# Optimization experiments

Measured on AMD Instinct MI355X. Metric: run time of the kernel, lower is better.

The kernel has to match this reference:

```python
import jax, jax.numpy as jnp
import numpy as np

V, E, G, D = 30000, 60000, 1200, 64
NODE_IN, EDGE_IN, EH = 74, 12, 128
N_MP, N_S2S, N_LSTM = 6, 6, 3


def setup_inputs() -> dict:
    key = jax.random.key(0)
    ks = iter(jax.random.split(key, 48))
    def rn(shape, s=0.05):
        return jax.random.normal(next(ks), shape, dtype=jnp.float32) * s
    inp = {
        "node_feats": jax.random.normal(next(ks), (V, NODE_IN), dtype=jnp.float32),
        "edge_feats": jax.random.normal(next(ks), (E, EDGE_IN), dtype=jnp.float32),
        "src": jax.random.randint(next(ks), (E,), 0, V, dtype=jnp.int32),
        "dst": jax.random.randint(next(ks), (E,), 0, V, dtype=jnp.int32),
        "node_graph_ids": jnp.sort(jax.random.randint(next(ks), (V,), 0, G, dtype=jnp.int32)),
        # MPNNGNN: node projection, edge network, NNConv bias, GRU
        "proj_W": rn((NODE_IN, D)), "proj_b": rn((D,)),
        "eW1": rn((EDGE_IN, EH)), "eb1": rn((EH,)),
        "eW2": rn((EH, D * D)), "eb2": rn((D * D,)),
        "conv_b": rn((D,)),
        "gru_Wih": rn((D, 3 * D)), "gru_bih": rn((3 * D,)),
        "gru_Whh": rn((D, 3 * D)), "gru_bhh": rn((3 * D,)),
        # process + predict MLPs
        "pW": rn((2 * D, D)), "pb": rn((D,)),
        "qW1": rn((D, D)), "qb1": rn((D,)),
        "qW2": rn((D, D)), "qb2": rn((D,)),
        "qW3": rn((D, 1)), "qb3": rn((1,)),
    }
    # Set2Set 3-layer LSTM: layer0 input 2D, layers 1-2 input D; gates i,f,g,o
    for l, din in enumerate([2 * D, D, D]):
        inp[f"lstm_Wih{l}"] = rn((din, 4 * D)); inp[f"lstm_bih{l}"] = rn((4 * D,))
        inp[f"lstm_Whh{l}"] = rn((D, 4 * D)); inp[f"lstm_bhh{l}"] = rn((4 * D,))
    return inp


def _forward(floats, src, dst, gids):
    (node_feats, edge_feats, proj_W, proj_b, eW1, eb1, eW2, eb2, conv_b,
     gru_Wih, gru_bih, gru_Whh, gru_bhh,
     lWih0, lbih0, lWhh0, lbhh0,
     lWih1, lbih1, lWhh1, lbhh1,
     lWih2, lbih2, lWhh2, lbhh2,
     pW, pb, qW1, qb1, qW2, qb2, qW3, qb3) = floats

    # ---- MPNNGNN ----
    h = jax.nn.relu(node_feats @ proj_W + proj_b)            # (V, D)
    hidden = h
    # per-edge weight matrices (edge_feats fixed across MP steps -> compute once)
    We = (jax.nn.relu(edge_feats @ eW1 + eb1) @ eW2 + eb2).reshape(E, D, D)
    for _ in range(N_MP):
        m = jnp.einsum('ei,eio->eo', h[src], We)             # (E, D)
        agg = jax.ops.segment_sum(m, dst, num_segments=V) + conv_b
        x = jax.nn.relu(agg)
        # PyTorch GRU cell
        gi = x @ gru_Wih + gru_bih
        gh = hidden @ gru_Whh + gru_bhh
        ir, iz, inn = jnp.split(gi, 3, axis=-1)
        hr, hz, hn = jnp.split(gh, 3, axis=-1)
        r = jax.nn.sigmoid(ir + hr)
        z = jax.nn.sigmoid(iz + hz)
        n = jnp.tanh(inn + r * hn)
        h = (1.0 - z) * n + z * hidden
        hidden = h

    # ---- Set2Set readout ----
    lstm = [(lWih0, lbih0, lWhh0, lbhh0),
            (lWih1, lbih1, lWhh1, lbhh1),
            (lWih2, lbih2, lWhh2, lbhh2)]
    hs = [jnp.zeros((G, D), h.dtype) for _ in range(N_LSTM)]
    cs = [jnp.zeros((G, D), h.dtype) for _ in range(N_LSTM)]
    q_star = jnp.zeros((G, 2 * D), h.dtype)
    for _ in range(N_S2S):
        x = q_star
        nhs, ncs = [], []
        for l, (Wih, bih, Whh, bhh) in enumerate(lstm):
            gates = x @ Wih + bih + hs[l] @ Whh + bhh
            i_g, f_g, g_g, o_g = jnp.split(gates, 4, axis=-1)
            c = jax.nn.sigmoid(f_g) * cs[l] + jax.nn.sigmoid(i_g) * jnp.tanh(g_g)
            hh = jax.nn.sigmoid(o_g) * jnp.tanh(c)
            nhs.append(hh); ncs.append(c)
            x = hh
        hs, cs = nhs, ncs
        q = x                                               # (G, D)
        e = jnp.sum(h * q[gids], axis=-1)                   # (V,)
        emax = jax.ops.segment_max(e, gids, num_segments=G, indices_are_sorted=True)
        ex = jnp.exp(e - emax[gids])
        denom = jax.ops.segment_sum(ex, gids, num_segments=G, indices_are_sorted=True)
        alpha = ex / denom[gids]                            # per-graph softmax
        readout = jax.ops.segment_sum(h * alpha[:, None], gids, num_segments=G, indices_are_sorted=True)
        q_star = jnp.concatenate([q, readout], axis=-1)     # (G, 2D)

    # ---- process + predict MLPs (dropout = identity in eval) ----
    gf = jax.nn.relu(q_star @ pW + pb)
    y = jax.nn.relu(gf @ qW1 + qb1)
    y = jax.nn.relu(y @ qW2 + qb2)
    return y @ qW3 + qb3                                    # (G, 1)


def reference(node_feats, edge_feats, src, dst, node_graph_ids,
              proj_W, proj_b, eW1, eb1, eW2, eb2, conv_b,
              gru_Wih, gru_bih, gru_Whh, gru_bhh,
              lstm_Wih0, lstm_bih0, lstm_Whh0, lstm_bhh0,
              lstm_Wih1, lstm_bih1, lstm_Whh1, lstm_bhh1,
              lstm_Wih2, lstm_bih2, lstm_Whh2, lstm_bhh2,
              pW, pb, qW1, qb1, qW2, qb2, qW3, qb3):
    floats = (node_feats, edge_feats, proj_W, proj_b, eW1, eb1, eW2, eb2, conv_b,
              gru_Wih, gru_bih, gru_Whh, gru_bhh,
              lstm_Wih0, lstm_bih0, lstm_Whh0, lstm_bhh0,
              lstm_Wih1, lstm_bih1, lstm_Whh1, lstm_bhh1,
              lstm_Wih2, lstm_bih2, lstm_Whh2, lstm_bhh2,
              pW, pb, qW1, qb1, qW2, qb2, qW3, qb3)
    return _forward(floats, src, dst, node_graph_ids)
```

## Files before the change

kernel.cpp:

```cpp
#include <hip/hip_runtime.h>
#include <stdint.h>
#include <math.h>

#define V 30000
#define E 60000
#define G 1200
#define D 64
#define NODE_IN 74
#define EDGE_IN 12
#define EH 128
#define N_MP 6
#define N_S2S 6

#define NBLK ((E + 63) / 64)
#define EPAD (NBLK * 64)
#define GRUBLK ((V + 31) / 32)

typedef short bf16x8 __attribute__((ext_vector_type(8)));
typedef float f32x4 __attribute__((ext_vector_type(4)));

__device__ __forceinline__ float sigmoidf_(float x) {
    return 1.0f / (1.0f + __expf(-x));
}
__device__ __forceinline__ float tanhf_(float x) {
    float t = __expf(-2.0f * fabsf(x));
    float r = (1.0f - t) / (1.0f + t);
    return copysignf(r, x);
}
__device__ __forceinline__ uint16_t f2bf(float f) {
    uint32_t u = __float_as_uint(f);
    u += 0x7fffu + ((u >> 16) & 1u);
    return (uint16_t)(u >> 16);
}
__device__ __forceinline__ float bf2f(uint16_t u) {
    return __uint_as_float(((uint32_t)u) << 16);
}

__global__ void k_zero(float* __restrict__ p, int n4) {
    int i = blockIdx.x * blockDim.x + threadIdx.x;
    if (i < n4) ((float4*)p)[i] = make_float4(0.f, 0.f, 0.f, 0.f);
}

__global__ void k_node_proj(const float* __restrict__ nf, const float* __restrict__ W,
                            const float* __restrict__ b, float* __restrict__ h) {
    int wave = threadIdx.x >> 6, lane = threadIdx.x & 63;
    int v = blockIdx.x * 4 + wave;
    __shared__ float xs[4][NODE_IN];
    xs[wave][lane] = nf[(size_t)v * NODE_IN + lane];
    if (lane + 64 < NODE_IN) xs[wave][lane + 64] = nf[(size_t)v * NODE_IN + lane + 64];
    __syncthreads();
    float acc = b[lane];
    #pragma unroll
    for (int i = 0; i < NODE_IN; ++i) acc = fmaf(xs[wave][i], W[i * D + lane], acc);
    h[(size_t)v * D + lane] = fmaxf(acc, 0.0f);
}

__global__ __launch_bounds__(256) void k_edge_hidden(const float* __restrict__ ef,
                              const float* __restrict__ W1,
                              const float* __restrict__ b1, uint16_t* __restrict__ HedgeP) {
    int blk = blockIdx.x;
    int t = threadIdx.x;
    int half = t >> 7, j = t & 127;
    __shared__ float xs[8][EDGE_IN];
    if (t < 8 * EDGE_IN) {
        int el = t / EDGE_IN, c = t % EDGE_IN;
        int e = blk * 8 + el;
        xs[el][c] = (e < E) ? ef[(size_t)e * EDGE_IN + c] : 0.f;
    }
    __syncthreads();
    #pragma unroll
    for (int l = 0; l < 4; ++l) {
        int el = half * 4 + l;
        int e = blk * 8 + el;
        float acc = b1[j];
        #pragma unroll
        for (int i = 0; i < EDGE_IN; ++i) acc = fmaf(xs[el][i], W1[i * EH + j], acc);
        float r = (e < E) ? fmaxf(acc, 0.0f) : 0.0f;
        int bb = e >> 6, ww = (e >> 4) & 3, m = e & 15;
        int kt = j >> 5, quad = (j >> 3) & 3, jj = j & 7;
        size_t off = ((((size_t)(bb * 4 + ww) * 4 + kt) * 4 + quad) * 16 + m) * 8 + jj;
        HedgeP[off] = f2bf(r);
    }
}

__global__ void k_prep_w2(const float* __restrict__ eW2, uint16_t* __restrict__ W2p) {
    int idx = blockIdx.x * 256 + threadIdx.x;
    int j = idx & 7;
    int n0 = (idx >> 3) & 15;
    int quad = (idx >> 7) & 3;
    int nt = (idx >> 9) & 3;
    int kt = (idx >> 11) & 3;
    int i = idx >> 13;
    int k = kt * 32 + quad * 8 + j;
    int col = i * 64 + nt * 16 + n0;
    W2p[idx] = f2bf(eW2[(size_t)k * 4096 + col]);
}

__global__ void k_prep_b2(const float* __restrict__ eb2, uint16_t* __restrict__ B2p) {
    int idx = blockIdx.x * 256 + threadIdx.x;
    if (idx >= 4096) { B2p[idx] = 0; return; }
    int j = idx & 7;
    int n0 = (idx >> 3) & 15;
    int quad = (idx >> 7) & 3;
    int nt = (idx >> 9) & 3;
    int kb = (idx >> 11) & 1;
    B2p[idx] = f2bf(eb2[(size_t)(kb * 32 + quad * 8 + j) * 64 + nt * 16 + n0]);
}

__global__ void k_prep_wc(const float* __restrict__ Wih, const float* __restrict__ Whh,
                          const float* __restrict__ bih, const float* __restrict__ bhh,
                          uint16_t* __restrict__ Wcp, float* __restrict__ bc) {
    int idx = blockIdx.x * 256 + threadIdx.x;
    int j = idx & 7;
    int n0 = (idx >> 3) & 15;
    int quad = (idx >> 7) & 3;
    int kt = (idx >> 9) & 3;
    int ot = idx >> 11;
    int k = kt * 32 + quad * 8 + j;
    int c = ot * 16 + n0;
    float val = 0.f;
    if (c < 128) {
        val = (k < 64) ? Wih[(size_t)k * 192 + c] : Whh[(size_t)(k - 64) * 192 + c];
    } else if (c < 192) {
        if (k < 64) val = Wih[(size_t)k * 192 + c];
    } else {
        if (k >= 64) val = Whh[(size_t)(k - 64) * 192 + (c - 64)];
    }
    Wcp[idx] = f2bf(val);
    if (idx < 256) {
        int d = idx & 63;
        float b;
        if (idx < 64)       b = bih[d] + bhh[d];
        else if (idx < 128) b = bih[64 + d] + bhh[64 + d];
        else if (idx < 192) b = bih[128 + d];
        else                b = bhh[128 + d];
        bc[idx] = b;
    }
}

__global__ __launch_bounds__(256, 3) void k_message_mfma(
    const uint16_t* __restrict__ HedgeP, const uint16_t* __restrict__ W2p,
    const uint16_t* __restrict__ B2p, const float* __restrict__ h,
    const int* __restrict__ src, const int* __restrict__ dst,
    float* __restrict__ agg) {
    const int bx = blockIdx.x;
    const int b = bx >> 1;
    const int ibase = (bx & 1) * 32;
    const int t = threadIdx.x;
    const int w = t >> 6, lane = t & 63;
    const int quad = lane >> 4, n0 = lane & 15;

    __shared__ uint16_t HsU[64][72];
    __shared__ int srcv[64], dstv[64];

    if (t < 64) {
        int e = b * 64 + t;
        int sv = 0, dv = -1;
        if (e < E) { sv = src[e]; dv = dst[e]; }
        srcv[t] = sv; dstv[t] = dv;
    }
    __syncthreads();
    for (int idx = t; idx < 4096; idx += 256) {
        int r = idx >> 6, c = idx & 63;
        HsU[r][c] = f2bf(h[(size_t)srcv[r] * 64 + c]);
    }
    bf16x8 Af[4][4];
    #pragma unroll
    for (int et = 0; et < 4; ++et)
        #pragma unroll
        for (int kt = 0; kt < 4; ++kt)
            Af[et][kt] = *(const bf16x8*)(HedgeP + (((size_t)(b * 4 + et) * 4 + kt) * 512) + lane * 8);
    __syncthreads();

    f32x4 acc[4];
    {
        const uint16_t* b2b = B2p + (size_t)ibase * 128;
        bf16x8 B2f0 = *(const bf16x8*)(b2b + (size_t)(0 * 4 + w) * 512 + lane * 8);
        bf16x8 B2f1 = *(const bf16x8*)(b2b + (size_t)(1 * 4 + w) * 512 + lane * 8);
        #pragma unroll
        for (int et = 0; et < 4; ++et) {
            bf16x8 hA0 = *(const bf16x8*)(&HsU[et * 16 + n0][quad * 8]);
            bf16x8 hA1 = *(const bf16x8*)(&HsU[et * 16 + n0][32 + quad * 8]);
            f32x4 z = {};
            z = __builtin_amdgcn_mfma_f32_16x16x32_bf16(hA0, B2f0, z, 0, 0, 0);
            acc[et] = __builtin_amdgcn_mfma_f32_16x16x32_bf16(hA1, B2f1, z, 0, 0, 0);
        }
    }

    for (int ii = 0; ii < 32; ++ii) {
        const int i = ibase + ii;
        const uint16_t* wb = W2p + (size_t)i * 8192 + lane * 8;
        bf16x8 Bf0 = *(const bf16x8*)(wb + (size_t)(0 * 4 + w) * 512);
        bf16x8 Bf1 = *(const bf16x8*)(wb + (size_t)(1 * 4 + w) * 512);
        bf16x8 Bf2 = *(const bf16x8*)(wb + (size_t)(2 * 4 + w) * 512);
        bf16x8 Bf3 = *(const bf16x8*)(wb + (size_t)(3 * 4 + w) * 512);
        #pragma unroll
        for (int et = 0; et < 4; ++et) {
            f32x4 tmp = {};
            tmp = __builtin_amdgcn_mfma_f32_16x16x32_bf16(Af[et][0], Bf0, tmp, 0, 0, 0);
            tmp = __builtin_amdgcn_mfma_f32_16x16x32_bf16(Af[et][1], Bf1, tmp, 0, 0, 0);
            tmp = __builtin_amdgcn_mfma_f32_16x16x32_bf16(Af[et][2], Bf2, tmp, 0, 0, 0);
            tmp = __builtin_amdgcn_mfma_f32_16x16x32_bf16(Af[et][3], Bf3, tmp, 0, 0, 0);
            int r0 = et * 16 + quad * 4;
            acc[et][0] = fmaf(bf2f(HsU[r0 + 0][i]), tmp[0], acc[et][0]);
            acc[et][1] = fmaf(bf2f(HsU[r0 + 1][i]), tmp[1], acc[et][1]);
            acc[et][2] = fmaf(bf2f(HsU[r0 + 2][i]), tmp[2], acc[et][2]);
            acc[et][3] = fmaf(bf2f(HsU[r0 + 3][i]), tmp[3], acc[et][3]);
        }
    }

    #pragma unroll
    for (int et = 0; et < 4; ++et) {
        #pragma unroll
        for (int reg = 0; reg < 4; ++reg) {
            int d = dstv[et * 16 + quad * 4 + reg];
            if (d >= 0)
                atomicAdd(agg + (size_t)d * 64 + w * 16 + n0, acc[et][reg]);
        }
    }
}

__global__ __launch_bounds__(256) void k_gru_mfma(
    float* __restrict__ agg, const float* __restrict__ convb,
    const uint16_t* __restrict__ Wcp, const float* __restrict__ bc,
    float* __restrict__ hcur) {
    const int blk = blockIdx.x;
    const int v0 = blk * 32;
    const int t = threadIdx.x;
    const int w = t >> 6, lane = t & 63;
    const int quad = lane >> 4, n0 = lane & 15;

    __shared__ uint16_t As[32][136];
    __shared__ uint16_t Gs[32][264];

    for (int idx = t; idx < 2048; idx += 256) {
        int r = idx >> 6, c = idx & 63;
        int v = v0 + r;
        if (v < V) {
            size_t off = (size_t)v * 64 + c;
            float x = fmaxf(agg[off] + convb[c], 0.f);
            agg[off] = 0.f;
            As[r][c] = f2bf(x);
            As[r][64 + c] = f2bf(hcur[off]);
        } else {
            As[r][c] = 0; As[r][64 + c] = 0;
        }
    }
    __syncthreads();

    bf16x8 Af[2][4];
    #pragma unroll
    for (int et = 0; et < 2; ++et)
        #pragma unroll
        for (int kt = 0; kt < 4; ++kt)
            Af[et][kt] = *(const bf16x8*)(&As[et * 16 + n0][kt * 32 + quad * 8]);

    f32x4 acc[2][4] = {};
    #pragma unroll
    for (int ot4 = 0; ot4 < 4; ++ot4) {
        const uint16_t* wb = Wcp + (size_t)((w * 4 + ot4) * 4) * 512 + lane * 8;
        bf16x8 B0 = *(const bf16x8*)(wb + 0 * 512);
        bf16x8 B1 = *(const bf16x8*)(wb + 1 * 512);
        bf16x8 B2 = *(const bf16x8*)(wb + 2 * 512);
        bf16x8 B3 = *(const bf16x8*)(wb + 3 * 512);
        #pragma unroll
        for (int et = 0; et < 2; ++et) {
            f32x4 a = acc[et][ot4];
            a = __builtin_amdgcn_mfma_f32_16x16x32_bf16(Af[et][0], B0, a, 0, 0, 0);
            a = __builtin_amdgcn_mfma_f32_16x16x32_bf16(Af[et][1], B1, a, 0, 0, 0);
            a = __builtin_amdgcn_mfma_f32_16x16x32_bf16(Af[et][2], B2, a, 0, 0, 0);
            a = __builtin_amdgcn_mfma_f32_16x16x32_bf16(Af[et][3], B3, a, 0, 0, 0);
            acc[et][ot4] = a;
        }
    }
    #pragma unroll
    for (int et = 0; et < 2; ++et)
        #pragma unroll
        for (int ot4 = 0; ot4 < 4; ++ot4)
            #pragma unroll
            for (int reg = 0; reg < 4; ++reg)
                Gs[et * 16 + quad * 4 + reg][(w * 4 + ot4) * 16 + n0] = f2bf(acc[et][ot4][reg]);
    __syncthreads();

    for (int idx = t; idx < 2048; idx += 256) {
        int r = idx >> 6, d = idx & 63;
        int v = v0 + r;
        if (v >= V) continue;
        size_t off = (size_t)v * 64 + d;
        float rp   = bf2f(Gs[r][d])        + bc[d];
        float zp   = bf2f(Gs[r][64 + d])   + bc[64 + d];
        float innv = bf2f(Gs[r][128 + d])  + bc[128 + d];
        float hnv  = bf2f(Gs[r][192 + d])  + bc[192 + d];
        float hv = hcur[off];
        float rr = sigmoidf_(rp);
        float zz = sigmoidf_(zp);
        float nn = tanhf_(innv + rr * hnv);
        hcur[off] = (1.f - zz) * nn + zz * hv;
    }
}

__global__ void k_seg(const int* __restrict__ gids, int* __restrict__ start) {
    int v = blockIdx.x * blockDim.x + threadIdx.x;
    if (v > V) return;
    int cur = (v < V) ? gids[v] : G;
    int prev = (v == 0) ? -1 : gids[v - 1];
    for (int g = prev + 1; g <= cur; ++g) start[g] = v;
}

#define LS_GPB 8
__global__ __launch_bounds__(256) void k_s2s_final(
    const float* __restrict__ h, const int* __restrict__ segs,
    const float* __restrict__ Wih0, const float* __restrict__ bih0,
    const float* __restrict__ Whh0, const float* __restrict__ bhh0,
    const float* __restrict__ Wih1, const float* __restrict__ bih1,
    const float* __restrict__ Whh1, const float* __restrict__ bhh1,
    const float* __restrict__ Wih2, const float* __restrict__ bih2,
    const float* __restrict__ Whh2, const float* __restrict__ bhh2,
    const float* __restrict__ pW, const float* __restrict__ pb,
    const float* __restrict__ qW1, const float* __restrict__ qb1,
    const float* __restrict__ qW2, const float* __restrict__ qb2,
    const float* __restrict__ qW3, const float* __restrict__ qb3,
    float* __restrict__ out) {
    const int g0 = blockIdx.x * LS_GPB;
    const int j = threadIdx.x;
    const int w = j >> 6, lane = j & 63;

    __shared__ float xs[LS_GPB][128];
    __shared__ float hsL[3][LS_GPB][64];
    __shared__ float csL[3][LS_GPB][64];
    __shared__ float gates[LS_GPB][256];
    __shared__ float qst[LS_GPB][128];

    for (int idx = j; idx < LS_GPB * 64 * 3; idx += 256) {
        ((float*)hsL)[idx] = 0.f;
        ((float*)csL)[idx] = 0.f;
    }
    for (int idx = j; idx < LS_GPB * 128; idx += 256) ((float*)qst)[idx] = 0.f;
    __syncthreads();

    const float* Wihs[3] = {Wih0, Wih1, Wih2};
    const float* bihs[3] = {bih0, bih1, bih2};
    const float* Whhs[3] = {Whh0, Whh1, Whh2};
    const float* bhhs[3] = {bhh0, bhh1, bhh2};
    const int dins[3] = {128, 64, 64};

    for (int s = 0; s < N_S2S; ++s) {
        for (int idx = j; idx < LS_GPB * 128; idx += 256) {
            int n = idx >> 7, d = idx & 127;
            xs[n][d] = qst[n][d];
        }
        __syncthreads();
        for (int l = 0; l < 3; ++l) {
            float acc[LS_GPB];
            float bsum = bihs[l][j] + bhhs[l][j];
            #pragma unroll
            for (int n = 0; n < LS_GPB; ++n) acc[n] = bsum;
            const float* Wih = Wihs[l];
            int din = dins[l];
            for (int i = 0; i < din; ++i) {
                float wv = Wih[i * 256 + j];
                #pragma unroll
                for (int n = 0; n < LS_GPB; ++n) acc[n] = fmaf(xs[n][i], wv, acc[n]);
            }
            const float* Whh = Whhs[l];
            for (int i = 0; i < 64; ++i) {
                float wv = Whh[i * 256 + j];
                #pragma unroll
                for (int n = 0; n < LS_GPB; ++n) acc[n] = fmaf(hsL[l][n][i], wv, acc[n]);
            }
            #pragma unroll
            for (int n = 0; n < LS_GPB; ++n) gates[n][j] = acc[n];
            __syncthreads();
            for (int idx = j; idx < LS_GPB * 64; idx += 256) {
                int n = idx >> 6, d = idx & 63;
                float ig = gates[n][d], fg = gates[n][64 + d];
                float gt = gates[n][128 + d], og = gates[n][192 + d];
                float c = sigmoidf_(fg) * csL[l][n][d] + sigmoidf_(ig) * tanhf_(gt);
                float hnew = sigmoidf_(og) * tanhf_(c);
                csL[l][n][d] = c;
                hsL[l][n][d] = hnew;
                xs[n][d] = hnew;
            }
            __syncthreads();
        }
        #pragma unroll
        for (int gi = 0; gi < 2; ++gi) {
            int gg = w + gi * 4;
            int g = g0 + gg;
            float qd = xs[gg][lane];
            int vs = segs[g], ve = segs[g + 1];
            float m = -INFINITY, sden = 0.f, accd = 0.f;
            for (int v = vs; v < ve; ++v) {
                float hv = h[(size_t)v * 64 + lane];
                float p = hv * qd;
                #pragma unroll
                for (int off = 32; off > 0; off >>= 1) p += __shfl_xor(p, off, 64);
                float nm = fmaxf(m, p);
                float e1 = __expf(m - nm);
                float e2 = __expf(p - nm);
                sden = sden * e1 + e2;
                accd = accd * e1 + hv * e2;
                m = nm;
            }
            float r = (ve > vs) ? accd / sden : 0.f;
            qst[gg][lane] = qd;
            qst[gg][64 + lane] = r;
        }
        __syncthreads();
    }

    #pragma unroll
    for (int gi = 0; gi < 2; ++gi) {
        int gg = w + gi * 4;
        int g = g0 + gg;
        float y = pb[lane];
        for (int i = 0; i < 128; ++i) y = fmaf(qst[gg][i], pW[i * 64 + lane], y);
        y = fmaxf(y, 0.f);
        gates[gg][lane] = y;
        float y1 = qb1[lane];
        for (int i = 0; i < 64; ++i) y1 = fmaf(gates[gg][i], qW1[i * 64 + lane], y1);
        y1 = fmaxf(y1, 0.f);
        gates[gg][64 + lane] = y1;
        float y2 = qb2[lane];
        for (int i = 0; i < 64; ++i) y2 = fmaf(gates[gg][64 + i], qW2[i * 64 + lane], y2);
        y2 = fmaxf(y2, 0.f);
        float p = y2 * qW3[lane];
        #pragma unroll
        for (int off = 32; off > 0; off >>= 1) p += __shfl_xor(p, off, 64);
        if (lane == 0) out[g] = p + qb3[0];
    }
}

extern "C" void kernel_launch(void* const* d_in, const int* in_sizes, int n_in,
                              void* d_out, int out_size, void* d_ws, size_t ws_size,
                              hipStream_t stream) {
    const float* node_feats = (const float*)d_in[0];
    const float* edge_feats = (const float*)d_in[1];
    const int*   src        = (const int*)d_in[2];
    const int*   dst        = (const int*)d_in[3];
    const int*   gids       = (const int*)d_in[4];
    const float* proj_W     = (const float*)d_in[5];
    const float* proj_b     = (const float*)d_in[6];
    const float* eW1        = (const float*)d_in[7];
    const float* eb1        = (const float*)d_in[8];
    const float* eW2        = (const float*)d_in[9];
    const float* eb2        = (const float*)d_in[10];
    const float* conv_b     = (const float*)d_in[11];
    const float* gru_Wih    = (const float*)d_in[12];
    const float* gru_bih    = (const float*)d_in[13];
    const float* gru_Whh    = (const float*)d_in[14];
    const float* gru_bhh    = (const float*)d_in[15];
    const float* pW         = (const float*)d_in[16];
    const float* pb         = (const float*)d_in[17];
    const float* qW1        = (const float*)d_in[18];
    const float* qb1        = (const float*)d_in[19];
    const float* qW2        = (const float*)d_in[20];
    const float* qb2        = (const float*)d_in[21];
    const float* qW3        = (const float*)d_in[22];
    const float* qb3        = (const float*)d_in[23];
    const float* lWih0 = (const float*)d_in[24]; const float* lbih0 = (const float*)d_in[25];
    const float* lWhh0 = (const float*)d_in[26]; const float* lbhh0 = (const float*)d_in[27];
    const float* lWih1 = (const float*)d_in[28]; const float* lbih1 = (const float*)d_in[29];
    const float* lWhh1 = (const float*)d_in[30]; const float* lbhh1 = (const float*)d_in[31];
    const float* lWih2 = (const float*)d_in[32]; const float* lbih2 = (const float*)d_in[33];
    const float* lWhh2 = (const float*)d_in[34]; const float* lbhh2 = (const float*)d_in[35];

    char* ws = (char*)d_ws;
    uint16_t* HedgeP = (uint16_t*)(ws + 0);
    uint16_t* W2p    = (uint16_t*)(ws + 15368192);
    uint16_t* B2p    = (uint16_t*)(ws + 16416768);
    float*    hcur   = (float*)(ws + 16433152);
    float*    agg    = (float*)(ws + 24113152);
    int*      segs   = (int*)(ws + 34557952);
    uint16_t* Wcp    = (uint16_t*)(ws + 32407552);
    float*    bc     = (float*)(ws + 32407552 + 65536);

    k_node_proj<<<V / 4, 256, 0, stream>>>(node_feats, proj_W, proj_b, hcur);
    k_edge_hidden<<<EPAD / 8, 256, 0, stream>>>(edge_feats, eW1, eb1, HedgeP);
    k_prep_w2<<<2048, 256, 0, stream>>>(eW2, W2p);
    k_prep_b2<<<32, 256, 0, stream>>>(eb2, B2p);
    k_prep_wc<<<128, 256, 0, stream>>>(gru_Wih, gru_Whh, gru_bih, gru_bhh, Wcp, bc);
    k_seg<<<(V + 1 + 255) / 256, 256, 0, stream>>>(gids, segs);
    k_zero<<<(480000 + 255) / 256, 256, 0, stream>>>(agg, 480000);

    for (int t = 0; t < N_MP; ++t) {
        k_message_mfma<<<NBLK * 2, 256, 0, stream>>>(HedgeP, W2p, B2p, hcur, src, dst, agg);
        k_gru_mfma<<<GRUBLK, 256, 0, stream>>>(agg, conv_b, Wcp, bc, hcur);
    }

    k_s2s_final<<<G / LS_GPB, 256, 0, stream>>>(hcur, segs,
        lWih0, lbih0, lWhh0, lbhh0,
        lWih1, lbih1, lWhh1, lbhh1,
        lWih2, lbih2, lWhh2, lbhh2,
        pW, pb, qW1, qb1, qW2, qb2, qW3, qb3,
        (float*)d_out);
}
```

Before: 954.0 us.

## Run Set2Set LSTM with one wavefront per graph using shuffles and packed gate weights

Rewrites the Set2Set/readout kernel to process one graph per 64-thread block. Each lane owns one hidden unit and computes all four LSTM gates from float4-packed weights that a new prep kernel interleaves. Inputs are broadcast with wave shuffles instead of shared memory, which removes block-wide syncs and lets 1200 blocks spread across the GPU instead of 150. The cost is that each graph re-reads the full LSTM weights with no reuse across graphs, so weight traffic per block rises.

```diff
diff --git a/kernel.cpp b/kernel.cpp
--- a/kernel.cpp
+++ b/kernel.cpp
@@ -138,6 +138,42 @@
     }
 }
 
+__global__ void k_prep_lstm(
+    const float* __restrict__ Wih0, const float* __restrict__ bih0,
+    const float* __restrict__ Whh0, const float* __restrict__ bhh0,
+    const float* __restrict__ Wih1, const float* __restrict__ bih1,
+    const float* __restrict__ Whh1, const float* __restrict__ bhh1,
+    const float* __restrict__ Wih2, const float* __restrict__ bih2,
+    const float* __restrict__ Whh2, const float* __restrict__ bhh2,
+    float4* __restrict__ WihP, float4* __restrict__ WhhP, float4* __restrict__ bc4) {
+    int idx = blockIdx.x * 256 + threadIdx.x;
+    if (idx < 16384) {
+        const float* W; int base;
+        if (idx < 8192)       { base = 0;     W = Wih0; }
+        else if (idx < 12288) { base = 8192;  W = Wih1; }
+        else                  { base = 12288; W = Wih2; }
+        int local = idx - base;
+        int i = local >> 6, d = local & 63;
+        WihP[idx] = make_float4(W[(size_t)i * 256 + d],       W[(size_t)i * 256 + 64 + d],
+                                W[(size_t)i * 256 + 128 + d], W[(size_t)i * 256 + 192 + d]);
+    } else if (idx < 28672) {
+        int li = idx - 16384;
+        int l = li >> 12;
+        int local = li & 4095;
+        int k = local >> 6, d = local & 63;
+        const float* W = (l == 0) ? Whh0 : (l == 1) ? Whh1 : Whh2;
+        WhhP[li] = make_float4(W[(size_t)k * 256 + d],       W[(size_t)k * 256 + 64 + d],
+                               W[(size_t)k * 256 + 128 + d], W[(size_t)k * 256 + 192 + d]);
+    } else if (idx < 28864) {
+        int bi = idx - 28672;
+        int l = bi >> 6, d = bi & 63;
+        const float* bi_ = (l == 0) ? bih0 : (l == 1) ? bih1 : bih2;
+        const float* bh_ = (l == 0) ? bhh0 : (l == 1) ? bhh1 : bhh2;
+        bc4[bi] = make_float4(bi_[d] + bh_[d],             bi_[64 + d] + bh_[64 + d],
+                              bi_[128 + d] + bh_[128 + d], bi_[192 + d] + bh_[192 + d]);
+    }
+}
+
 __global__ __launch_bounds__(256, 3) void k_message_mfma(
     const uint16_t* __restrict__ HedgeP, const uint16_t* __restrict__ W2p,
     const uint16_t* __restrict__ B2p, const float* __restrict__ h,
@@ -307,128 +343,122 @@
     for (int g = prev + 1; g <= cur; ++g) start[g] = v;
 }
 
-#define LS_GPB 8
-__global__ __launch_bounds__(256) void k_s2s_final(
+__global__ __launch_bounds__(64) void k_s2s_final(
     const float* __restrict__ h, const int* __restrict__ segs,
-    const float* __restrict__ Wih0, const float* __restrict__ bih0,
-    const float* __restrict__ Whh0, const float* __restrict__ bhh0,
-    const float* __restrict__ Wih1, const float* __restrict__ bih1,
-    const float* __restrict__ Whh1, const float* __restrict__ bhh1,
-    const float* __restrict__ Wih2, const float* __restrict__ bih2,
-    const float* __restrict__ Whh2, const float* __restrict__ bhh2,
+    const float4* __restrict__ WihP, const float4* __restrict__ WhhP,
+    const float4* __restrict__ bc4,
     const float* __restrict__ pW, const float* __restrict__ pb,
     const float* __restrict__ qW1, const float* __restrict__ qb1,
     const float* __restrict__ qW2, const float* __restrict__ qb2,
     const float* __restrict__ qW3, const float* __restrict__ qb3,
     float* __restrict__ out) {
-    const int g0 = blockIdx.x * LS_GPB;
-    const int j = threadIdx.x;
-    const int w = j >> 6, lane = j & 63;
-
-    __shared__ float xs[LS_GPB][128];
-    __shared__ float hsL[3][LS_GPB][64];
-    __shared__ float csL[3][LS_GPB][64];
-    __shared__ float gates[LS_GPB][256];
-    __shared__ float qst[LS_GPB][128];
-
-    for (int idx = j; idx < LS_GPB * 64 * 3; idx += 256) {
-        ((float*)hsL)[idx] = 0.f;
-        ((float*)csL)[idx] = 0.f;
-    }
-    for (int idx = j; idx < LS_GPB * 128; idx += 256) ((float*)qst)[idx] = 0.f;
-    __syncthreads();
-
-    const float* Wihs[3] = {Wih0, Wih1, Wih2};
-    const float* bihs[3] = {bih0, bih1, bih2};
-    const float* Whhs[3] = {Whh0, Whh1, Whh2};
-    const float* bhhs[3] = {bhh0, bhh1, bhh2};
-    const int dins[3] = {128, 64, 64};
+    const int g = blockIdx.x;
+    const int lane = threadIdx.x;
+    const int vs = segs[g], ve = segs[g + 1];
+
+    float h0 = 0.f, c0 = 0.f, h1 = 0.f, c1 = 0.f, h2 = 0.f, c2 = 0.f;
+    float qlo = 0.f, qhi = 0.f;
+    const float4 b0 = bc4[lane], b1 = bc4[64 + lane], b2 = bc4[128 + lane];
+    const float4* Wih1p = WihP + 8192;
+    const float4* Wih2p = WihP + 12288;
+    const float4* Whh1p = WhhP + 4096;
+    const float4* Whh2p = WhhP + 8192;
 
     for (int s = 0; s < N_S2S; ++s) {
-        for (int idx = j; idx < LS_GPB * 128; idx += 256) {
-            int n = idx >> 7, d = idx & 127;
-            xs[n][d] = qst[n][d];
-        }
-        __syncthreads();
-        for (int l = 0; l < 3; ++l) {
-            float acc[LS_GPB];
-            float bsum = bihs[l][j] + bhhs[l][j];
+        float4 a = b0;
+        #pragma unroll 8
+        for (int i = 0; i < 64; ++i) {
+            float xv = __shfl(qlo, i, 64);
+            float4 wv = WihP[i * 64 + lane];
+            a.x = fmaf(xv, wv.x, a.x); a.y = fmaf(xv, wv.y, a.y);
+            a.z = fmaf(xv, wv.z, a.z); a.w = fmaf(xv, wv.w, a.w);
+        }
+        #pragma unroll 8
+        for (int i = 0; i < 64; ++i) {
+            float xv = __shfl(qhi, i, 64);
+            float4 wv = WihP[(64 + i) * 64 + lane];
+            a.x = fmaf(xv, wv.x, a.x); a.y = fmaf(xv, wv.y, a.y);
+            a.z = fmaf(xv, wv.z, a.z); a.w = fmaf(xv, wv.w, a.w);
+        }
+        #pragma unroll 8
+        for (int k = 0; k < 64; ++k) {
+            float hv = __shfl(h0, k, 64);
+            float4 wv = WhhP[k * 64 + lane];
+            a.x = fmaf(hv, wv.x, a.x); a.y = fmaf(hv, wv.y, a.y);
+            a.z = fmaf(hv, wv.z, a.z); a.w = fmaf(hv, wv.w, a.w);
+        }
+        c0 = sigmoidf_(a.y) * c0 + sigmoidf_(a.x) * tanhf_(a.z);
+        h0 = sigmoidf_(a.w) * tanhf_(c0);
+        a = b1;
+        #pragma unroll 8
+        for (int i = 0; i < 64; ++i) {
+            float xv = __shfl(h0, i, 64);
+            float4 wv = Wih1p[i * 64 + lane];
+            a.x = fmaf(xv, wv.x, a.x); a.y = fmaf(xv, wv.y, a.y);
+            a.z = fmaf(xv, wv.z, a.z); a.w = fmaf(xv, wv.w, a.w);
+        }
+        #pragma unroll 8
+        for (int k = 0; k < 64; ++k) {
+            float hv = __shfl(h1, k, 64);
+            float4 wv = Whh1p[k * 64 + lane];
+            a.x = fmaf(hv, wv.x, a.x); a.y = fmaf(hv, wv.y, a.y);
+            a.z = fmaf(hv, wv.z, a.z); a.w = fmaf(hv, wv.w, a.w);
+        }
+        c1 = sigmoidf_(a.y) * c1 + sigmoidf_(a.x) * tanhf_(a.z);
+        h1 = sigmoidf_(a.w) * tanhf_(c1);
+        a = b2;
+        #pragma unroll 8
+        for (int i = 0; i < 64; ++i) {
+            float xv = __shfl(h1, i, 64);
+            float4 wv = Wih2p[i * 64 + lane];
+            a.x = fmaf(xv, wv.x, a.x); a.y = fmaf(xv, wv.y, a.y);
+            a.z = fmaf(xv, wv.z, a.z); a.w = fmaf(xv, wv.w, a.w);
+        }
+        #pragma unroll 8
+        for (int k = 0; k < 64; ++k) {
+            float hv = __shfl(h2, k, 64);
+            float4 wv = Whh2p[k * 64 + lane];
+            a.x = fmaf(hv, wv.x, a.x); a.y = fmaf(hv, wv.y, a.y);
+            a.z = fmaf(hv, wv.z, a.z); a.w = fmaf(hv, wv.w, a.w);
+        }
+        c2 = sigmoidf_(a.y) * c2 + sigmoidf_(a.x) * tanhf_(a.z);
+        h2 = sigmoidf_(a.w) * tanhf_(c2);
+        float qd = h2;
+        float m = -INFINITY, sden = 0.f, accd = 0.f;
+        for (int v = vs; v < ve; ++v) {
+            float hv = h[(size_t)v * 64 + lane];
+            float p = hv * qd;
             #pragma unroll
-            for (int n = 0; n < LS_GPB; ++n) acc[n] = bsum;
-            const float* Wih = Wihs[l];
-            int din = dins[l];
-            for (int i = 0; i < din; ++i) {
-                float wv = Wih[i * 256 + j];
-                #pragma unroll
-                for (int n = 0; n < LS_GPB; ++n) acc[n] = fmaf(xs[n][i], wv, acc[n]);
-            }
-            const float* Whh = Whhs[l];
-            for (int i = 0; i < 64; ++i) {
-                float wv = Whh[i * 256 + j];
-                #pragma unroll
-                for (int n = 0; n < LS_GPB; ++n) acc[n] = fmaf(hsL[l][n][i], wv, acc[n]);
-            }
-            #pragma unroll
-            for (int n = 0; n < LS_GPB; ++n) gates[n][j] = acc[n];
-            __syncthreads();
-            for (int idx = j; idx < LS_GPB * 64; idx += 256) {
-                int n = idx >> 6, d = idx & 63;
-                float ig = gates[n][d], fg = gates[n][64 + d];
-                float gt = gates[n][128 + d], og = gates[n][192 + d];
-                float c = sigmoidf_(fg) * csL[l][n][d] + sigmoidf_(ig) * tanhf_(gt);
-                float hnew = sigmoidf_(og) * tanhf_(c);
-                csL[l][n][d] = c;
-                hsL[l][n][d] = hnew;
-                xs[n][d] = hnew;
-            }
-            __syncthreads();
-        }
-        #pragma unroll
-        for (int gi = 0; gi < 2; ++gi) {
-            int gg = w + gi * 4;
-            int g = g0 + gg;
-            float qd = xs[gg][lane];
-            int vs = segs[g], ve = segs[g + 1];
-            float m = -INFINITY, sden = 0.f, accd = 0.f;
-            for (int v = vs; v < ve; ++v) {
-                float hv = h[(size_t)v * 64 + lane];
-                float p = hv * qd;
-                #pragma unroll
-                for (int off = 32; off > 0; off >>= 1) p += __shfl_xor(p, off, 64);
-                float nm = fmaxf(m, p);
-                float e1 = __expf(m - nm);
-                float e2 = __expf(p - nm);
-                sden = sden * e1 + e2;
-                accd = accd * e1 + hv * e2;
-                m = nm;
-            }
-            float r = (ve > vs) ? accd / sden : 0.f;
-            qst[gg][lane] = qd;
-            qst[gg][64 + lane] = r;
-        }
-        __syncthreads();
-    }
-
-    #pragma unroll
-    for (int gi = 0; gi < 2; ++gi) {
-        int gg = w + gi * 4;
-        int g = g0 + gg;
-        float y = pb[lane];
-        for (int i = 0; i < 128; ++i) y = fmaf(qst[gg][i], pW[i * 64 + lane], y);
-        y = fmaxf(y, 0.f);
-        gates[gg][lane] = y;
-        float y1 = qb1[lane];
-        for (int i = 0; i < 64; ++i) y1 = fmaf(gates[gg][i], qW1[i * 64 + lane], y1);
-        y1 = fmaxf(y1, 0.f);
-        gates[gg][64 + lane] = y1;
-        float y2 = qb2[lane];
-        for (int i = 0; i < 64; ++i) y2 = fmaf(gates[gg][64 + i], qW2[i * 64 + lane], y2);
-        y2 = fmaxf(y2, 0.f);
-        float p = y2 * qW3[lane];
-        #pragma unroll
-        for (int off = 32; off > 0; off >>= 1) p += __shfl_xor(p, off, 64);
-        if (lane == 0) out[g] = p + qb3[0];
-    }
+            for (int off = 32; off > 0; off >>= 1) p += __shfl_xor(p, off, 64);
+            float nm = fmaxf(m, p);
+            float e1 = __expf(m - nm);
+            float e2 = __expf(p - nm);
+            sden = sden * e1 + e2;
+            accd = fmaf(hv, e2, accd * e1);
+            m = nm;
+        }
+        qlo = qd;
+        qhi = (ve > vs) ? accd / sden : 0.f;
+    }
+
+    float y = pb[lane];
+    #pragma unroll 8
+    for (int i = 0; i < 64; ++i) y = fmaf(__shfl(qlo, i, 64), pW[i * 64 + lane], y);
+    #pragma unroll 8
+    for (int i = 0; i < 64; ++i) y = fmaf(__shfl(qhi, i, 64), pW[(64 + i) * 64 + lane], y);
+    y = fmaxf(y, 0.f);
+    float y1 = qb1[lane];
+    #pragma unroll 8
+    for (int i = 0; i < 64; ++i) y1 = fmaf(__shfl(y, i, 64), qW1[i * 64 + lane], y1);
+    y1 = fmaxf(y1, 0.f);
+    float y2 = qb2[lane];
+    #pragma unroll 8
+    for (int i = 0; i < 64; ++i) y2 = fmaf(__shfl(y1, i, 64), qW2[i * 64 + lane], y2);
+    y2 = fmaxf(y2, 0.f);
+    float p = y2 * qW3[lane];
+    #pragma unroll
+    for (int off = 32; off > 0; off >>= 1) p += __shfl_xor(p, off, 64);
+    if (lane == 0) out[g] = p + qb3[0];
 }
 
 extern "C" void kernel_launch(void* const* d_in, const int* in_sizes, int n_in,
@@ -474,12 +504,19 @@
     int*      segs   = (int*)(ws + 34557952);
     uint16_t* Wcp    = (uint16_t*)(ws + 32407552);
     float*    bc     = (float*)(ws + 32407552 + 65536);
+    float4*   WihP   = (float4*)(ws + 33329152);
+    float4*   WhhP   = (float4*)(ws + 33591296);
+    float4*   bc4    = (float4*)(ws + 33787904);
 
     k_node_proj<<<V / 4, 256, 0, stream>>>(node_feats, proj_W, proj_b, hcur);
     k_edge_hidden<<<EPAD / 8, 256, 0, stream>>>(edge_feats, eW1, eb1, HedgeP);
     k_prep_w2<<<2048, 256, 0, stream>>>(eW2, W2p);
     k_prep_b2<<<32, 256, 0, stream>>>(eb2, B2p);
     k_prep_wc<<<128, 256, 0, stream>>>(gru_Wih, gru_Whh, gru_bih, gru_bhh, Wcp, bc);
+    k_prep_lstm<<<113, 256, 0, stream>>>(lWih0, lbih0, lWhh0, lbhh0,
+                                         lWih1, lbih1, lWhh1, lbhh1,
+                                         lWih2, lbih2, lWhh2, lbhh2,
+                                         WihP, WhhP, bc4);
     k_seg<<<(V + 1 + 255) / 256, 256, 0, stream>>>(gids, segs);
     k_zero<<<(480000 + 255) / 256, 256, 0, stream>>>(agg, 480000);
 
@@ -488,10 +525,7 @@
         k_gru_mfma<<<GRUBLK, 256, 0, stream>>>(agg, conv_b, Wcp, bc, hcur);
     }
 
-    k_s2s_final<<<G / LS_GPB, 256, 0, stream>>>(hcur, segs,
-        lWih0, lbih0, lWhh0, lbhh0,
-        lWih1, lbih1, lWhh1, lbhh1,
-        lWih2, lbih2, lWhh2, lbhh2,
+    k_s2s_final<<<G, 64, 0, stream>>>(hcur, segs, WihP, WhhP, bc4,
         pW, pb, qW1, qb1, qW2, qb2, qW3, qb3,
         (float*)d_out);
 }
```

After: 857.0 us, median of 3. 10.2% less time.
